# Kernel tuning notes

Hardware: AMD Instinct MI355X
Metric: run time of the kernel (lower is better)

## Reference

```python
import jax, jax.numpy as jnp
import numpy as np

C = 32  # input multiplicity per irrep (0e and 1o)
D = 32  # output multiplicity per irrep


def pe_inputs(x):
    # x: [B, 2, 3, F]; permutation-equivariant pooled channels
    x_self = x
    x_flavor = x.sum(axis=2, keepdims=True) - x_self
    x_nunubar = x.sum(axis=1, keepdims=True) - x_self
    x_all = x.sum(axis=(1, 2), keepdims=True) - x_self - x_flavor - x_nunubar
    x_flavor = x_flavor / (x.shape[2] - 1)
    x_nunubar = x_nunubar / (x.shape[1] - 1)
    x_all = x_all / ((x.shape[1] - 1) * (x.shape[2] - 1))
    return x_self, x_flavor, x_nunubar, x_all


def _split(x):
    # irreps '32x0e + 32x1o': first C scalars, then C vectors flattened (C,3)
    s = x[..., :C]
    v = x[..., C:].reshape(x.shape[:-1] + (C, 3))
    return s, v


def fctp(x1, x2, W):
    # e3nn FullyConnectedTensorProduct('Cx0e+Cx1o', 'Cx0e+Cx1o', 'Dx0e+Dx1o')
    # W: [4, C, C, D] stacked path weights: [ss->s, vv->s, sv->v, vs->v]
    s1, v1 = _split(x1)
    s2, v2 = _split(x2)
    norm = 1.0 / (C * np.sqrt(2.0))  # sqrt(dim(ir_out) / fan), fan = 2*C^2
    inv_sqrt3 = 1.0 / np.sqrt(3.0)   # wigner_3j(1,1,0) = delta_ij/sqrt(3)
    y_s = norm * (jnp.einsum('uvw,...u,...v->...w', W[0], s1, s2)
                  + inv_sqrt3 * jnp.einsum('uvw,...ui,...vi->...w', W[1], v1, v2))
    y_v = norm * (jnp.einsum('uvw,...u,...vk->...wk', W[2], s1, v2)
                  + jnp.einsum('uvw,...uk,...v->...wk', W[3], v1, s2))
    return jnp.concatenate([y_s, y_v.reshape(y_v.shape[:-2] + (3 * D,))], axis=-1)


def setup_inputs() -> dict:
    key = jax.random.key(0)
    ks = jax.random.split(key, 5)
    B = 16384
    x = jax.random.normal(ks[0], (B, 2, 3, C + 3 * C), dtype=jnp.float32)
    W_self = jax.random.normal(ks[1], (4, C, C, D), dtype=jnp.float32)
    W_flavor = jax.random.normal(ks[2], (4, C, C, D), dtype=jnp.float32)
    W_nunubar = jax.random.normal(ks[3], (4, C, C, D), dtype=jnp.float32)
    W_all = jax.random.normal(ks[4], (4, C, C, D), dtype=jnp.float32)
    return {"x": x, "W_self": W_self, "W_flavor": W_flavor,
            "W_nunubar": W_nunubar, "W_all": W_all}


def reference(x, W_self, W_flavor, W_nunubar, W_all):
    xs, xf, xn, xa = pe_inputs(x)
    y = (fctp(xs, xs, W_self)
         + fctp(xf, xf, W_flavor)
         + fctp(xn, xn, W_nunubar)
         + fctp(xa, xa, W_all))
    return y
```

## Files before the change

kernel.cpp:

```cpp
#include <hip/hip_runtime.h>


typedef _Float16 half8 __attribute__((ext_vector_type(8)));
typedef float   float4_t __attribute__((ext_vector_type(4)));

#define NORM 0.022097086912079608f
#define INV_SQRT3 0.5773502691896258f
#define FS 98

__global__ void prep_kernel(const float* __restrict__ Wa, const float* __restrict__ Wb,
                            const float* __restrict__ Wc, const float* __restrict__ Wd,
                            _Float16* __restrict__ B1s, _Float16* __restrict__ B2s) {
    const float* Ws[4] = {Wa, Wb, Wc, Wd};
    int idx = blockIdx.x * 256 + threadIdx.x;
    if (idx < 262144) {
        int j    = idx & 7;
        int lane = (idx >> 3) & 63;
        int h    = (idx >> 9) & 1;
        int s    = (idx >> 10) & 3;
        int ch   = (idx >> 12) & 15;
        int t    = idx >> 16;
        int m = lane & 15, q = lane >> 4;
        int n = h * 16 + m;
        int k = ch * 128 + s * 32 + q * 8 + j;
        int seg = k >> 10, u = (k >> 5) & 31, v = k & 31;
        const float* W = Ws[t];
        float val;
        if (seg == 0) val = NORM * W[0 * 32768 + u * 1024 + v * 32 + n];
        else          val = NORM * INV_SQRT3 * W[1 * 32768 + u * 1024 + v * 32 + n];
        B1s[idx] = (_Float16)val;
    } else {
        int idx2 = idx - 262144;
        if (idx2 < 131072) {
            int j    = idx2 & 7;
            int lane = (idx2 >> 3) & 63;
            int h    = (idx2 >> 9) & 1;
            int s2   = (idx2 >> 10) & 1;
            int ch   = (idx2 >> 11) & 15;
            int t    = idx2 >> 15;
            int m = lane & 15, q = lane >> 4;
            int n = h * 16 + m;
            int k = ch * 64 + s2 * 32 + q * 8 + j;
            int u = k >> 5, v = k & 31;
            const float* W = Ws[t];
            float val = NORM * (W[2 * 32768 + u * 1024 + v * 32 + n] +
                                W[3 * 32768 + v * 1024 + u * 32 + n]);
            B2s[idx2] = (_Float16)val;
        }
    }
}

__launch_bounds__(192, 3)
__global__ void petp_main(const float* __restrict__ x,
                          const _Float16* __restrict__ B1s,
                          const _Float16* __restrict__ B2s,
                          float* __restrict__ y) {
    __shared__ _Float16 featT[128 * FS];

    const int tid  = threadIdx.x;
    const int wave = tid / 64;
    const int lane = tid & 63;
    const int m = lane & 15;
    const int q = lane >> 4;
    const int wg = blockIdx.x;
    const int pbase = wave * 32;

    float4_t acc_s[2][2];
    float4_t acc_v[6][2];
    float4_t zero = {0.f, 0.f, 0.f, 0.f};
#pragma unroll
    for (int i = 0; i < 2; ++i) { acc_s[i][0] = zero; acc_s[i][1] = zero; }
#pragma unroll
    for (int i = 0; i < 6; ++i) { acc_v[i][0] = zero; acc_v[i][1] = zero; }

    const float* xg = x + (size_t)wg * (96 * 128);

#pragma unroll 1
    for (int t = 0; t < 4; ++t) {
        __syncthreads();
#pragma unroll 1
        for (int it = 0; it < 11; ++it) {
            int item = it * 192 + tid;
            if (item < 2048) {
                int b = item >> 7;
                int c = item & 127;
                const float* bp = xg + b * 768 + c;
                float v00 = bp[0],   v01 = bp[128], v02 = bp[256];
                float v10 = bp[384], v11 = bp[512], v12 = bp[640];
                float rs0 = v00 + v01 + v02, rs1 = v10 + v11 + v12;
                float cs0 = v00 + v10, cs1 = v01 + v11, cs2 = v02 + v12;
                float tot = rs0 + rs1;
                float xv[6] = {v00, v01, v02, v10, v11, v12};
                float rs[2] = {rs0, rs1};
                float cs[3] = {cs0, cs1, cs2};
                int row;
                if (c < 32) row = c;
                else { int cc = c - 32; row = 32 + (cc % 3) * 32 + (cc / 3); }
#pragma unroll
                for (int p6 = 0; p6 < 6; ++p6) {
                    int i = p6 / 3, j = p6 % 3;
                    float xvv = xv[p6];
                    float f;
                    if      (t == 0) f = xvv;
                    else if (t == 1) f = (rs[i] - xvv) * 0.5f;
                    else if (t == 2) f = cs[j] - xvv;
                    else             f = (tot - rs[i] - cs[j] + xvv) * 0.5f;
                    int posL = b * 6 + p6;
                    featT[row * FS + posL] = (_Float16)f;
                }
            }
        }
        __syncthreads();

        half8 p_ss[2];
        half8 p_v[2][3];
#pragma unroll
        for (int tl = 0; tl < 2; ++tl) {
            int posL = pbase + tl * 16 + m;
#pragma unroll
            for (int j = 0; j < 8; ++j)
                p_ss[tl][j] = featT[(q * 8 + j) * FS + posL];
#pragma unroll
            for (int i = 0; i < 3; ++i)
#pragma unroll
                for (int j = 0; j < 8; ++j)
                    p_v[tl][i][j] = featT[(32 + i * 32 + q * 8 + j) * FS + posL];
        }

        const _Float16* B1w = B1s + t * 65536 + lane * 8;
        const _Float16* B2w = B2s + t * 32768 + lane * 8;

#pragma unroll 1
        for (int ch = 0; ch < 16; ++ch) {
            if (ch < 8) {
#pragma unroll
                for (int s = 0; s < 4; ++s) {
                    int u = ch * 4 + s;
                    half8 bf0 = *(const half8*)(B1w + ((ch * 4 + s) * 2 + 0) * 512);
                    half8 bf1 = *(const half8*)(B1w + ((ch * 4 + s) * 2 + 1) * 512);
#pragma unroll
                    for (int tl = 0; tl < 2; ++tl) {
                        int posL = pbase + tl * 16 + m;
                        _Float16 bc = featT[u * FS + posL];
                        half8 af = p_ss[tl] * bc;
                        acc_s[tl][0] = __builtin_amdgcn_mfma_f32_16x16x32_f16(af, bf0, acc_s[tl][0], 0, 0, 0);
                        acc_s[tl][1] = __builtin_amdgcn_mfma_f32_16x16x32_f16(af, bf1, acc_s[tl][1], 0, 0, 0);
                    }
                }
            } else {
#pragma unroll
                for (int s = 0; s < 4; ++s) {
                    int u = (ch - 8) * 4 + s;
                    half8 bf0 = *(const half8*)(B1w + ((ch * 4 + s) * 2 + 0) * 512);
                    half8 bf1 = *(const half8*)(B1w + ((ch * 4 + s) * 2 + 1) * 512);
#pragma unroll
                    for (int tl = 0; tl < 2; ++tl) {
                        int posL = pbase + tl * 16 + m;
                        _Float16 g0 = featT[(32 + u) * FS + posL];
                        _Float16 g1 = featT[(64 + u) * FS + posL];
                        _Float16 g2 = featT[(96 + u) * FS + posL];
                        half8 af = p_v[tl][0] * g0 + p_v[tl][1] * g1 + p_v[tl][2] * g2;
                        acc_s[tl][0] = __builtin_amdgcn_mfma_f32_16x16x32_f16(af, bf0, acc_s[tl][0], 0, 0, 0);
                        acc_s[tl][1] = __builtin_amdgcn_mfma_f32_16x16x32_f16(af, bf1, acc_s[tl][1], 0, 0, 0);
                    }
                }
            }
#pragma unroll
            for (int s2 = 0; s2 < 2; ++s2) {
                int u = ch * 2 + s2;
                half8 bf0 = *(const half8*)(B2w + ((ch * 2 + s2) * 2 + 0) * 512);
                half8 bf1 = *(const half8*)(B2w + ((ch * 2 + s2) * 2 + 1) * 512);
                _Float16 bcs[2];
#pragma unroll
                for (int sub = 0; sub < 2; ++sub)
                    bcs[sub] = featT[u * FS + pbase + sub * 16 + m];
#pragma unroll
                for (int tv = 0; tv < 6; ++tv) {
                    int sub = tv & 1, kc = tv >> 1;
                    half8 af = p_v[sub][kc] * bcs[sub];
                    acc_v[tv][0] = __builtin_amdgcn_mfma_f32_16x16x32_f16(af, bf0, acc_v[tv][0], 0, 0, 0);
                    acc_v[tv][1] = __builtin_amdgcn_mfma_f32_16x16x32_f16(af, bf1, acc_v[tv][1], 0, 0, 0);
                }
            }
        }
    }

    float* yg = y + (size_t)wg * (96 * 128);
#pragma unroll
    for (int tl = 0; tl < 2; ++tl) {
#pragma unroll
        for (int nh = 0; nh < 2; ++nh) {
            int w = nh * 16 + m;
#pragma unroll
            for (int r = 0; r < 4; ++r) {
                int pos = wave * 32 + tl * 16 + q * 4 + r;
                yg[pos * 128 + w] = acc_s[tl][nh][r];
            }
        }
    }
#pragma unroll
    for (int tv = 0; tv < 6; ++tv) {
        int sub = tv & 1, kc = tv >> 1;
#pragma unroll
        for (int nh = 0; nh < 2; ++nh) {
            int w = nh * 16 + m;
#pragma unroll
            for (int r = 0; r < 4; ++r) {
                int pos = wave * 32 + sub * 16 + q * 4 + r;
                yg[pos * 128 + 32 + 3 * w + kc] = acc_v[tv][nh][r];
            }
        }
    }
}

extern "C" void kernel_launch(void* const* d_in, const int* in_sizes, int n_in,
                              void* d_out, int out_size, void* d_ws, size_t ws_size,
                              hipStream_t stream) {
    const float* x  = (const float*)d_in[0];
    const float* Wa = (const float*)d_in[1];
    const float* Wb = (const float*)d_in[2];
    const float* Wc = (const float*)d_in[3];
    const float* Wd = (const float*)d_in[4];
    float* y = (float*)d_out;

    _Float16* B1s = (_Float16*)d_ws;
    _Float16* B2s = B1s + 262144;

    int nbatch = in_sizes[0] / 768;
    int nwg = nbatch / 16;

    prep_kernel<<<(262144 + 131072) / 256, 256, 0, stream>>>(Wa, Wb, Wc, Wd, B1s, B2s);
    petp_main<<<nwg, 192, 0, stream>>>(x, B1s, B2s, y);
}
```

Before: 241.1 us.

## Switch to 32x32x16 MFMA with row-major LDS features and repacked weights

```diff
diff --git a/kernel.cpp b/kernel.cpp
--- a/kernel.cpp
+++ b/kernel.cpp
@@ -2,11 +2,11 @@
 
 
 typedef _Float16 half8 __attribute__((ext_vector_type(8)));
-typedef float   float4_t __attribute__((ext_vector_type(4)));
+typedef float  floatx16 __attribute__((ext_vector_type(16)));
 
 #define NORM 0.022097086912079608f
 #define INV_SQRT3 0.5773502691896258f
-#define FS 98
+#define FR 136
 
 __global__ void prep_kernel(const float* __restrict__ Wa, const float* __restrict__ Wb,
                             const float* __restrict__ Wc, const float* __restrict__ Wd,
@@ -16,13 +16,10 @@
     if (idx < 262144) {
         int j    = idx & 7;
         int lane = (idx >> 3) & 63;
-        int h    = (idx >> 9) & 1;
-        int s    = (idx >> 10) & 3;
-        int ch   = (idx >> 12) & 15;
+        int f    = (idx >> 9) & 127;
         int t    = idx >> 16;
-        int m = lane & 15, q = lane >> 4;
-        int n = h * 16 + m;
-        int k = ch * 128 + s * 32 + q * 8 + j;
+        int n = lane & 31;
+        int k = f * 16 + (lane >> 5) * 8 + j;
         int seg = k >> 10, u = (k >> 5) & 31, v = k & 31;
         const float* W = Ws[t];
         float val;
@@ -34,13 +31,10 @@
         if (idx2 < 131072) {
             int j    = idx2 & 7;
             int lane = (idx2 >> 3) & 63;
-            int h    = (idx2 >> 9) & 1;
-            int s2   = (idx2 >> 10) & 1;
-            int ch   = (idx2 >> 11) & 15;
+            int f    = (idx2 >> 9) & 63;
             int t    = idx2 >> 15;
-            int m = lane & 15, q = lane >> 4;
-            int n = h * 16 + m;
-            int k = ch * 64 + s2 * 32 + q * 8 + j;
+            int n = lane & 31;
+            int k = f * 16 + (lane >> 5) * 8 + j;
             int u = k >> 5, v = k & 31;
             const float* W = Ws[t];
             float val = NORM * (W[2 * 32768 + u * 1024 + v * 32 + n] +
@@ -50,28 +44,26 @@
     }
 }
 
-__launch_bounds__(192, 3)
+__launch_bounds__(192, 2)
 __global__ void petp_main(const float* __restrict__ x,
                           const _Float16* __restrict__ B1s,
                           const _Float16* __restrict__ B2s,
                           float* __restrict__ y) {
-    __shared__ _Float16 featT[128 * FS];
+    __shared__ _Float16 feat[96 * FR];
 
     const int tid  = threadIdx.x;
     const int wave = tid / 64;
     const int lane = tid & 63;
-    const int m = lane & 15;
-    const int q = lane >> 4;
+    const int n32 = lane & 31;
+    const int q2  = lane >> 5;
     const int wg = blockIdx.x;
     const int pbase = wave * 32;
+    const int pos = pbase + n32;
 
-    float4_t acc_s[2][2];
-    float4_t acc_v[6][2];
-    float4_t zero = {0.f, 0.f, 0.f, 0.f};
+    floatx16 acc_s = {0.f};
+    floatx16 acc_v[3];
 #pragma unroll
-    for (int i = 0; i < 2; ++i) { acc_s[i][0] = zero; acc_s[i][1] = zero; }
-#pragma unroll
-    for (int i = 0; i < 6; ++i) { acc_v[i][0] = zero; acc_v[i][1] = zero; }
+    for (int i = 0; i < 3; ++i) acc_v[i] = acc_s;
 
     const float* xg = x + (size_t)wg * (96 * 128);
 
@@ -93,9 +85,9 @@
                 float xv[6] = {v00, v01, v02, v10, v11, v12};
                 float rs[2] = {rs0, rs1};
                 float cs[3] = {cs0, cs1, cs2};
-                int row;
-                if (c < 32) row = c;
-                else { int cc = c - 32; row = 32 + (cc % 3) * 32 + (cc / 3); }
+                int col;
+                if (c < 32) col = c;
+                else { int cc = c - 32; col = 32 + (cc % 3) * 32 + (cc / 3); }
 #pragma unroll
                 for (int p6 = 0; p6 < 6; ++p6) {
                     int i = p6 / 3, j = p6 % 3;
@@ -106,110 +98,74 @@
                     else if (t == 2) f = cs[j] - xvv;
                     else             f = (tot - rs[i] - cs[j] + xvv) * 0.5f;
                     int posL = b * 6 + p6;
-                    featT[row * FS + posL] = (_Float16)f;
+                    feat[posL * FR + col] = (_Float16)f;
                 }
             }
         }
         __syncthreads();
 
+        const _Float16* fr = &feat[pos * FR];
+        half8 s_all[4];
+        half8 v_all[3][4];
+#pragma unroll
+        for (int j4 = 0; j4 < 4; ++j4) s_all[j4] = *(const half8*)(fr + j4 * 8);
+#pragma unroll
+        for (int i = 0; i < 3; ++i)
+#pragma unroll
+            for (int j4 = 0; j4 < 4; ++j4)
+                v_all[i][j4] = *(const half8*)(fr + 32 + i * 32 + j4 * 8);
         half8 p_ss[2];
-        half8 p_v[2][3];
+        half8 p_v[3][2];
 #pragma unroll
-        for (int tl = 0; tl < 2; ++tl) {
-            int posL = pbase + tl * 16 + m;
-#pragma unroll
-            for (int j = 0; j < 8; ++j)
-                p_ss[tl][j] = featT[(q * 8 + j) * FS + posL];
+        for (int h = 0; h < 2; ++h) {
+            p_ss[h] = *(const half8*)(fr + h * 16 + q2 * 8);
 #pragma unroll
             for (int i = 0; i < 3; ++i)
-#pragma unroll
-                for (int j = 0; j < 8; ++j)
-                    p_v[tl][i][j] = featT[(32 + i * 32 + q * 8 + j) * FS + posL];
+                p_v[i][h] = *(const half8*)(fr + 32 + i * 32 + h * 16 + q2 * 8);
         }
 
-        const _Float16* B1w = B1s + t * 65536 + lane * 8;
-        const _Float16* B2w = B2s + t * 32768 + lane * 8;
+        const _Float16* B1v = B1s + t * 65536 + lane * 8;
+        const _Float16* B2v = B2s + t * 32768 + lane * 8;
 
-#pragma unroll 1
-        for (int ch = 0; ch < 16; ++ch) {
-            if (ch < 8) {
 #pragma unroll
-                for (int s = 0; s < 4; ++s) {
-                    int u = ch * 4 + s;
-                    half8 bf0 = *(const half8*)(B1w + ((ch * 4 + s) * 2 + 0) * 512);
-                    half8 bf1 = *(const half8*)(B1w + ((ch * 4 + s) * 2 + 1) * 512);
+        for (int ku = 0; ku < 32; ++ku) {
+            half8 c1a = *(const half8*)(B1v + (2 * ku + 0) * 512);
+            half8 c1b = *(const half8*)(B1v + (2 * ku + 1) * 512);
+            half8 c2a = *(const half8*)(B2v + (2 * ku + 0) * 512);
+            half8 c2b = *(const half8*)(B2v + (2 * ku + 1) * 512);
+            _Float16 bc = s_all[ku >> 3][ku & 7];
+            acc_s = __builtin_amdgcn_mfma_f32_32x32x16_f16(p_ss[0] * bc, c1a, acc_s, 0, 0, 0);
+            acc_s = __builtin_amdgcn_mfma_f32_32x32x16_f16(p_ss[1] * bc, c1b, acc_s, 0, 0, 0);
 #pragma unroll
-                    for (int tl = 0; tl < 2; ++tl) {
-                        int posL = pbase + tl * 16 + m;
-                        _Float16 bc = featT[u * FS + posL];
-                        half8 af = p_ss[tl] * bc;
-                        acc_s[tl][0] = __builtin_amdgcn_mfma_f32_16x16x32_f16(af, bf0, acc_s[tl][0], 0, 0, 0);
-                        acc_s[tl][1] = __builtin_amdgcn_mfma_f32_16x16x32_f16(af, bf1, acc_s[tl][1], 0, 0, 0);
-                    }
-                }
-            } else {
+            for (int kc = 0; kc < 3; ++kc) {
+                acc_v[kc] = __builtin_amdgcn_mfma_f32_32x32x16_f16(p_v[kc][0] * bc, c2a, acc_v[kc], 0, 0, 0);
+                acc_v[kc] = __builtin_amdgcn_mfma_f32_32x32x16_f16(p_v[kc][1] * bc, c2b, acc_v[kc], 0, 0, 0);
+            }
+        }
 #pragma unroll
-                for (int s = 0; s < 4; ++s) {
-                    int u = (ch - 8) * 4 + s;
-                    half8 bf0 = *(const half8*)(B1w + ((ch * 4 + s) * 2 + 0) * 512);
-                    half8 bf1 = *(const half8*)(B1w + ((ch * 4 + s) * 2 + 1) * 512);
-#pragma unroll
-                    for (int tl = 0; tl < 2; ++tl) {
-                        int posL = pbase + tl * 16 + m;
-                        _Float16 g0 = featT[(32 + u) * FS + posL];
-                        _Float16 g1 = featT[(64 + u) * FS + posL];
-                        _Float16 g2 = featT[(96 + u) * FS + posL];
-                        half8 af = p_v[tl][0] * g0 + p_v[tl][1] * g1 + p_v[tl][2] * g2;
-                        acc_s[tl][0] = __builtin_amdgcn_mfma_f32_16x16x32_f16(af, bf0, acc_s[tl][0], 0, 0, 0);
-                        acc_s[tl][1] = __builtin_amdgcn_mfma_f32_16x16x32_f16(af, bf1, acc_s[tl][1], 0, 0, 0);
-                    }
-                }
-            }
-#pragma unroll
-            for (int s2 = 0; s2 < 2; ++s2) {
-                int u = ch * 2 + s2;
-                half8 bf0 = *(const half8*)(B2w + ((ch * 2 + s2) * 2 + 0) * 512);
-                half8 bf1 = *(const half8*)(B2w + ((ch * 2 + s2) * 2 + 1) * 512);
-                _Float16 bcs[2];
-#pragma unroll
-                for (int sub = 0; sub < 2; ++sub)
-                    bcs[sub] = featT[u * FS + pbase + sub * 16 + m];
-#pragma unroll
-                for (int tv = 0; tv < 6; ++tv) {
-                    int sub = tv & 1, kc = tv >> 1;
-                    half8 af = p_v[sub][kc] * bcs[sub];
-                    acc_v[tv][0] = __builtin_amdgcn_mfma_f32_16x16x32_f16(af, bf0, acc_v[tv][0], 0, 0, 0);
-                    acc_v[tv][1] = __builtin_amdgcn_mfma_f32_16x16x32_f16(af, bf1, acc_v[tv][1], 0, 0, 0);
-                }
-            }
+        for (int ku = 0; ku < 32; ++ku) {
+            half8 g1a = *(const half8*)(B1v + (64 + 2 * ku + 0) * 512);
+            half8 g1b = *(const half8*)(B1v + (64 + 2 * ku + 1) * 512);
+            _Float16 b0 = v_all[0][ku >> 3][ku & 7];
+            _Float16 b1 = v_all[1][ku >> 3][ku & 7];
+            _Float16 b2 = v_all[2][ku >> 3][ku & 7];
+            half8 af0 = p_v[0][0] * b0 + p_v[1][0] * b1 + p_v[2][0] * b2;
+            half8 af1 = p_v[0][1] * b0 + p_v[1][1] * b1 + p_v[2][1] * b2;
+            acc_s = __builtin_amdgcn_mfma_f32_32x32x16_f16(af0, g1a, acc_s, 0, 0, 0);
+            acc_s = __builtin_amdgcn_mfma_f32_32x32x16_f16(af1, g1b, acc_s, 0, 0, 0);
         }
     }
 
     float* yg = y + (size_t)wg * (96 * 128);
+    const int w = n32;
 #pragma unroll
-    for (int tl = 0; tl < 2; ++tl) {
+    for (int r = 0; r < 16; ++r) {
+        int row = (r & 3) + 8 * (r >> 2) + 4 * q2;
+        int p = pbase + row;
+        yg[p * 128 + w] = acc_s[r];
 #pragma unroll
-        for (int nh = 0; nh < 2; ++nh) {
-            int w = nh * 16 + m;
-#pragma unroll
-            for (int r = 0; r < 4; ++r) {
-                int pos = wave * 32 + tl * 16 + q * 4 + r;
-                yg[pos * 128 + w] = acc_s[tl][nh][r];
-            }
-        }
-    }
-#pragma unroll
-    for (int tv = 0; tv < 6; ++tv) {
-        int sub = tv & 1, kc = tv >> 1;
-#pragma unroll
-        for (int nh = 0; nh < 2; ++nh) {
-            int w = nh * 16 + m;
-#pragma unroll
-            for (int r = 0; r < 4; ++r) {
-                int pos = wave * 32 + sub * 16 + q * 4 + r;
-                yg[pos * 128 + 32 + 3 * w + kc] = acc_v[tv][nh][r];
-            }
-        }
+        for (int kc = 0; kc < 3; ++kc)
+            yg[p * 128 + 32 + 3 * w + kc] = acc_v[kc][r];
     }
 }
 
```

Measured after the change: 321.9 us. 33.5% more time.
